# Kernel optimization log

Hardware: AMD Instinct MI355X
Metric: run time of the kernel (lower is better)

Reference implementation:

```python
import jax, jax.numpy as jnp
import numpy as np

B = 256
NUM_PRIMARY = 32      # cfg.num_primary_caps
PRIM_ATOMS = 8
NUM_CLASSES = 10
DIGIT_ATOMS = 16
NUM_ROUTING = 3       # cfg.num_routing (DigitCap)
IN_DIM = 6 * 6 * NUM_PRIMARY  # 1152
NUM_PIXELS = 28 * 28 * 1


def squash(s, axis):
    # v = ||s||^2/(1+||s||^2) * s/||s||
    n2 = jnp.sum(jnp.square(s), axis=axis, keepdims=True)
    return s * (n2 / (1.0 + n2)) / jnp.sqrt(n2 + 1e-9)


def conv2d(x, w, stride):
    return jax.lax.conv_general_dilated(
        x, w, (stride, stride), 'VALID',
        dimension_numbers=('NCHW', 'OIHW', 'NCHW'))


def setup_inputs() -> dict:
    key = jax.random.key(0)
    ks = jax.random.split(key, 10)
    x = jax.random.uniform(ks[0], (B, 1, 28, 28), jnp.float32)
    labels = jax.random.randint(ks[1], (B,), 0, NUM_CLASSES)
    y = jax.nn.one_hot(labels, NUM_CLASSES, dtype=jnp.float32)
    conv1_w = 0.05 * jax.random.normal(ks[2], (256, 1, 9, 9), jnp.float32)
    conv1_b = jnp.full((256,), 0.1, jnp.float32)
    # primary capsule conv: 256 -> 32 caps * 8 atoms, k=9, s=2 (bias applied after routing)
    prim_w = 0.05 * jax.random.normal(ks[3], (NUM_PRIMARY * PRIM_ATOMS, 256, 9, 9), jnp.float32)
    prim_b = jnp.full((NUM_PRIMARY, PRIM_ATOMS), 0.1, jnp.float32)
    # digit capsule transform: [in_dim, in_atoms, out_dim, out_atoms]
    digit_w = 0.05 * jax.random.normal(ks[4], (IN_DIM, PRIM_ATOMS, NUM_CLASSES, DIGIT_ATOMS), jnp.float32)
    digit_b = jnp.full((NUM_CLASSES, DIGIT_ATOMS), 0.1, jnp.float32)
    w1 = 0.05 * jax.random.normal(ks[5], (NUM_CLASSES * DIGIT_ATOMS, 512), jnp.float32)
    b1 = jnp.zeros((512,), jnp.float32)
    w2 = 0.05 * jax.random.normal(ks[6], (512, 1024), jnp.float32)
    b2 = jnp.zeros((1024,), jnp.float32)
    w3 = 0.05 * jax.random.normal(ks[7], (1024, NUM_PIXELS), jnp.float32)
    b3 = jnp.zeros((NUM_PIXELS,), jnp.float32)
    return dict(x=x, y=y, conv1_w=conv1_w, conv1_b=conv1_b, prim_w=prim_w,
                prim_b=prim_b, digit_w=digit_w, digit_b=digit_b,
                w1=w1, b1=b1, w2=w2, b2=b2, w3=w3, b3=b3)


def reference(x, y, conv1_w, conv1_b, prim_w, prim_b, digit_w, digit_b,
              w1, b1, w2, b2, w3, b3):
    # conv stem
    h = jax.nn.relu(conv2d(x, conv1_w, 1) + conv1_b[None, :, None, None])  # [B,256,20,20]

    # PrimaryCap: conv votes [B, in_dim=1, out=32, atoms=8, 6, 6]; num_routing=1
    votes_p = conv2d(h, prim_w, 2).reshape(B, NUM_PRIMARY, PRIM_ATOMS, 6, 6)
    # one routing iter, input_dim=1: softmax(zeros) over output_dim -> uniform 1/32
    preact_p = votes_p / NUM_PRIMARY + prim_b[None, :, :, None, None]
    caps1 = squash(preact_p, axis=2)  # [B,32,8,6,6]

    # permute(0,1,3,4,2) then flatten -> [B, 1152, 8]
    x3 = jnp.transpose(caps1, (0, 1, 3, 4, 2)).reshape(B, IN_DIM, PRIM_ATOMS)

    # DigitCap votes: [B, in_dim, out_dim, out_atoms]
    votes = jnp.einsum('bia,iaot->biot', x3, digit_w)
    logits = jnp.zeros((B, IN_DIM, NUM_CLASSES), votes.dtype)
    act = None
    for _ in range(NUM_ROUTING):
        route = jax.nn.softmax(logits, axis=2)  # over output capsules
        preact = jnp.einsum('bio,biot->bot', route, votes) + digit_b
        act = squash(preact, axis=-1)  # [B,10,16]
        logits = logits + jnp.einsum('biot,bot->bio', votes, act)
    digit = act

    # Reconstruction: mask by label, 160 -> 512 -> 1024 -> 784
    masked = (digit * y[:, :, None]).reshape(B, NUM_CLASSES * DIGIT_ATOMS)
    r = jax.nn.relu(masked @ w1 + b1)
    r = jax.nn.relu(r @ w2 + b2)
    recon = jax.nn.sigmoid(r @ w3 + b3)
    return digit, recon
```

## Files before the change

kernel.cpp:

```cpp
#include <hip/hip_runtime.h>
#include <hip/hip_bf16.h>

typedef unsigned short u16;
typedef unsigned int u32;

static __device__ __forceinline__ float us2f(u16 u) {
    return __uint_as_float(((u32)u) << 16);
}
static __device__ __forceinline__ u16 f2bu(float f) {
    u32 u = __float_as_uint(f);
    return (u16)((u + 0x7fffu + ((u >> 16) & 1u)) >> 16);
}

typedef __attribute__((ext_vector_type(8))) __bf16 bf16x8;
typedef __attribute__((ext_vector_type(4))) float f32x4;

static __device__ __forceinline__ void async16(const u16* g, u16* l) {
    __builtin_amdgcn_global_load_lds(
        (const __attribute__((address_space(1))) unsigned int*)g,
        (__attribute__((address_space(3))) unsigned int*)l, 16, 0, 0);
}

__global__ void fill_sentinel(float* out, int n, float val) {
    int g = blockIdx.x * 256 + threadIdx.x;
    if (g < n) out[g] = val;
}

__global__ __launch_bounds__(256) void conv_c1wb(const float* __restrict__ w,
                                                 u16* __restrict__ wb)
{
    const int j = blockIdx.x, c = threadIdx.x;
    wb[j * 256 + c] = f2bu(w[c * 81 + j]);
}

__global__ __launch_bounds__(256) void conv1_kernel(const float* __restrict__ x,
    const u16* __restrict__ wb, const float* __restrict__ bias, u16* __restrict__ h)
{
    __shared__ float xs[784];
    __shared__ u16 wl[81 * 256];
    const int b = blockIdx.x >> 2, g = blockIdx.x & 3;
    const int c = threadIdx.x;
    for (int idx = c; idx < 784; idx += 256) xs[idx] = x[b * 784 + idx];
    for (int idx = c; idx < 20736; idx += 256) wl[idx] = wb[idx];
    __syncthreads();
    const float bv = bias[c];
    #pragma unroll 1
    for (int iy = g * 5; iy < g * 5 + 5; ++iy) {
        float acc[20];
        #pragma unroll
        for (int i = 0; i < 20; ++i) acc[i] = bv;
        #pragma unroll 1
        for (int dy = 0; dy < 9; ++dy) {
            float xr[28];
            const float4* xrow = reinterpret_cast<const float4*>(&xs[(iy + dy) * 28]);
            #pragma unroll
            for (int i = 0; i < 7; ++i) {
                float4 v = xrow[i];
                xr[4*i] = v.x; xr[4*i+1] = v.y; xr[4*i+2] = v.z; xr[4*i+3] = v.w;
            }
            #pragma unroll
            for (int dx = 0; dx < 9; ++dx) {
                const float wv = us2f(wl[(dy * 9 + dx) * 256 + c]);
                #pragma unroll
                for (int ix = 0; ix < 20; ++ix) acc[ix] += xr[ix + dx] * wv;
            }
        }
        u16* hp = h + ((b * 20 + iy) * 20) * 256 + c;
        #pragma unroll
        for (int ix = 0; ix < 20; ++ix) hp[ix * 256] = f2bu(fmaxf(acc[ix], 0.f));
    }
}

__global__ __launch_bounds__(256) void transpose_primw(const float* __restrict__ w,
                                                       u16* __restrict__ wt)
{
    __shared__ u16 wl[81 * 258];
    const int n = blockIdx.x, tid = threadIdx.x;
    const float* ws = w + (size_t)n * 20736;
    for (int idx = tid; idx < 20736; idx += 256) {
        const int cc = idx / 81, kk = idx - cc * 81;
        wl[kk * 258 + cc] = f2bu(ws[idx]);
    }
    __syncthreads();
    u16* wo = wt + (size_t)n * 20736;
    for (int q = tid; q < 20736; q += 256)
        wo[q] = wl[(q >> 8) * 258 + (q & 255)];
}

__global__ __launch_bounds__(256) void conv_dwb(const float* __restrict__ dw,
                                                u16* __restrict__ dwb_t)
{
    const int g = blockIdx.x * 256 + threadIdx.x;
    dwb_t[g] = f2bu(dw[g]);
}

__global__ __launch_bounds__(256, 2) void prim_gemm_split(const u16* __restrict__ h,
    const u16* __restrict__ wT, float* __restrict__ pm)
{
    __shared__ u16 As[3 * 4096];
    __shared__ u16 Bs[3 * 8192];
    const int tid = threadIdx.x;
    const int split = blockIdx.y;
    const int mBase = blockIdx.x * 128;
    const int lane = tid & 63, wv = tid >> 6;
    const int swzq = (tid & 3) ^ ((lane >> 3) & 3);
    const int rA = wv * 32 + (lane >> 2);
    const int rB = wv * 64 + (lane >> 2);
    int mA0 = mBase + rA;
    int bA0 = mA0 / 36, rr0 = mA0 % 36;
    const int aBase0 = ((bA0 * 20 + 2 * (rr0 / 6)) * 20 + 2 * (rr0 % 6)) * 256 + swzq * 8;
    int mA1 = mA0 + 16;
    int bA1 = mA1 / 36, rr1 = mA1 % 36;
    const int aBase1 = ((bA1 * 20 + 2 * (rr1 / 6)) * 20 + 2 * (rr1 % 6)) * 256 + swzq * 8;
    const u16* bp0 = wT + (size_t)rB * 20736 + swzq * 8;

    int kglob = split * 3456;
    int ky = kglob / 2304; int krem = kglob - ky * 2304;
    int kx = krem >> 8; int c0 = krem & 255;

    f32x4 acc[4][8];
    #pragma unroll
    for (int i = 0; i < 4; ++i)
        #pragma unroll
        for (int j = 0; j < 8; ++j) acc[i][j] = (f32x4){0.f, 0.f, 0.f, 0.f};

    const int wm = wv >> 1, wn = wv & 1;
    const int lcol = lane & 15, lquad = lane >> 4;
    const int rswz = (lquad ^ ((lcol >> 1) & 3)) * 8;
    const u16* Arow = As + (wm * 64 + lcol) * 32 + rswz;
    const u16* Brow = Bs + (wn * 128 + lcol) * 32 + rswz;
    u16* aD = As + wv * 1024;
    u16* bD = Bs + wv * 2048;

    #define STAGE(sel)  do {                                                   \
        const int koffA = (ky * 20 + kx) * 256 + c0;                           \
        async16(h + aBase0 + koffA, aD + (sel) * 4096);                        \
        async16(h + aBase1 + koffA, aD + (sel) * 4096 + 512);                  \
        async16(bp0 + kglob,          bD + (sel) * 8192);                      \
        async16(bp0 + 331776 + kglob, bD + (sel) * 8192 + 512);               \
        async16(bp0 + 663552 + kglob, bD + (sel) * 8192 + 1024);              \
        async16(bp0 + 995328 + kglob, bD + (sel) * 8192 + 1536);              \
        kglob += 32; c0 += 32;                                                 \
        if (c0 == 256) { c0 = 0; if (++kx == 9) { kx = 0; ++ky; } }            \
    } while (0)

    #define COMPUTE(sel)  do {                                                 \
        const u16* Ab = Arow + (sel) * 4096;                                   \
        const u16* Bb = Brow + (sel) * 8192;                                   \
        bf16x8 af[4], bfr[8];                                                  \
        _Pragma("unroll")                                                      \
        for (int i = 0; i < 4; ++i)                                            \
            af[i] = *reinterpret_cast<const bf16x8*>(Ab + i * 512);            \
        _Pragma("unroll")                                                      \
        for (int j = 0; j < 8; ++j)                                            \
            bfr[j] = *reinterpret_cast<const bf16x8*>(Bb + j * 512);           \
        __builtin_amdgcn_s_setprio(1);                                         \
        _Pragma("unroll")                                                      \
        for (int i = 0; i < 4; ++i)                                            \
            _Pragma("unroll")                                                  \
            for (int j = 0; j < 8; ++j)                                        \
                acc[i][j] = __builtin_amdgcn_mfma_f32_16x16x32_bf16(af[i], bfr[j], acc[i][j], 0, 0, 0); \
        __builtin_amdgcn_s_setprio(0);                                         \
    } while (0)

    STAGE(0);
    STAGE(1);
    int cb = 0, sb = 2;
    #pragma unroll 1
    for (int kt = 0; kt < 106; ++kt) {
        STAGE(sb);
        asm volatile("s_waitcnt vmcnt(12)" ::: "memory");
        __builtin_amdgcn_s_barrier();
        __builtin_amdgcn_sched_barrier(0);
        COMPUTE(cb);
        __builtin_amdgcn_sched_barrier(0);
        __builtin_amdgcn_s_barrier();
        __builtin_amdgcn_sched_barrier(0);
        cb = (cb == 2) ? 0 : cb + 1;
        sb = (sb == 2) ? 0 : sb + 1;
    }
    asm volatile("s_waitcnt vmcnt(6)" ::: "memory");
    __builtin_amdgcn_s_barrier();
    __builtin_amdgcn_sched_barrier(0);
    COMPUTE(1);
    __builtin_amdgcn_sched_barrier(0);
    asm volatile("s_waitcnt vmcnt(0)" ::: "memory");
    __builtin_amdgcn_s_barrier();
    __builtin_amdgcn_sched_barrier(0);
    COMPUTE(2);
    #undef STAGE
    #undef COMPUTE

    #pragma unroll
    for (int i = 0; i < 4; ++i) {
        const int mrow = mBase + wm * 64 + i * 16 + lquad * 4;
        #pragma unroll
        for (int j = 0; j < 8; ++j) {
            const int ncol = wn * 128 + j * 16 + lcol;
            #pragma unroll
            for (int r = 0; r < 4; ++r)
                unsafeAtomicAdd(&pm[(size_t)(mrow + r) * 256 + ncol], acc[i][j][r]);
        }
    }
}

__global__ __launch_bounds__(256) void squash_kernel(float* __restrict__ pm,
    const float* __restrict__ pb)
{
    const int m = blockIdx.x, t = threadIdx.x;
    float pre = pm[(size_t)m * 256 + t] * (1.f / 32.f) + pb[t];
    float sq = pre * pre;
    sq += __shfl_xor(sq, 1); sq += __shfl_xor(sq, 2); sq += __shfl_xor(sq, 4);
    float scale = (sq / (1.f + sq)) * rsqrtf(sq + 1e-9f);
    pm[(size_t)m * 256 + t] = pre * scale;
}

__global__ __launch_bounds__(192) void votes_gemm(const float* __restrict__ x3m,
    const u16* __restrict__ dwb_t, u16* __restrict__ votes, int hb)
{
    __shared__ float dws[8 * 1280];
    __shared__ float x3s[64 * 64];
    const int ic = blockIdx.x * 8, bc = blockIdx.y * 64;
    const int tid = threadIdx.x;
    for (int q = tid; q < 10240; q += 192)
        dws[q] = us2f(dwb_t[(size_t)ic * 1280 + q]);
    for (int q = tid; q < 4096; q += 192) {
        const int b_l = q >> 6, r = q & 63, i_l = r >> 3, a = r & 7;
        const int i = ic + i_l, cap = i / 36, p = i - cap * 36;
        x3s[q] = x3m[((size_t)(hb + bc + b_l) * 36 + p) * 256 + cap * 8 + a];
    }
    __syncthreads();
    if (tid < 160) {
        const int ot = tid;
        float dwr[8][8];
        #pragma unroll
        for (int i_l = 0; i_l < 8; ++i_l)
            #pragma unroll
            for (int a = 0; a < 8; ++a)
                dwr[i_l][a] = dws[i_l * 1280 + a * 160 + ot];
        #pragma unroll 1
        for (int b_l = 0; b_l < 64; ++b_l) {
            u16 ob[8];
            #pragma unroll
            for (int i_l = 0; i_l < 8; ++i_l) {
                const float* xp = &x3s[b_l * 64 + i_l * 8];
                float v = 0.f;
                #pragma unroll
                for (int a = 0; a < 8; ++a) v += xp[a] * dwr[i_l][a];
                ob[i_l] = f2bu(v);
            }
            uint4 o4;
            o4.x = (u32)ob[0] | ((u32)ob[1] << 16);
            o4.y = (u32)ob[2] | ((u32)ob[3] << 16);
            o4.z = (u32)ob[4] | ((u32)ob[5] << 16);
            o4.w = (u32)ob[6] | ((u32)ob[7] << 16);
            *reinterpret_cast<uint4*>(&votes[((size_t)(bc + b_l) * 160 + ot) * 1152 + ic]) = o4;
        }
    }
}

__global__ __launch_bounds__(256) void routing_act3(const u16* __restrict__ votes,
    const float* __restrict__ logits, float* __restrict__ preactD, int hb, int uniform)
{
    __shared__ float route_s[384 * 10];
    __shared__ float vs[160 * 65];
    const int ic = blockIdx.x * 384, b_l = blockIdx.y;
    const int gb = hb + b_l;
    const int tid = threadIdx.x;
    if (!uniform) {
        for (int q = tid; q < 384; q += 256) {
            const float* lg = &logits[((size_t)gb * 1152 + ic + q) * 10];
            float l[10]; float mx = -1e30f;
            #pragma unroll
            for (int k = 0; k < 10; ++k) { l[k] = lg[k]; mx = fmaxf(mx, l[k]); }
            float s = 0.f;
            #pragma unroll
            for (int k = 0; k < 10; ++k) { l[k] = __expf(l[k] - mx); s += l[k]; }
            const float inv = 1.f / s;
            #pragma unroll
            for (int k = 0; k < 10; ++k) route_s[q * 10 + k] = l[k] * inv;
        }
    }
    float acc = 0.f;
    const int o = (tid & 255) >> 4;
    #pragma unroll 1
    for (int sc = 0; sc < 6; ++sc) {
        __syncthreads();
        for (int q = tid; q < 1280; q += 256) {
            const int ot = q >> 3, i8 = q & 7;
            const uint4 d = *reinterpret_cast<const uint4*>(
                &votes[((size_t)b_l * 160 + ot) * 1152 + ic + sc * 64 + i8 * 8]);
            const u32 du[4] = {d.x, d.y, d.z, d.w};
            float* vp = &vs[ot * 65 + i8 * 8];
            #pragma unroll
            for (int k = 0; k < 4; ++k) {
                vp[2 * k]     = __uint_as_float(du[k] << 16);
                vp[2 * k + 1] = __uint_as_float(du[k] & 0xffff0000u);
            }
        }
        __syncthreads();
        if (tid < 160) {
            const float* vrow = &vs[tid * 65];
            if (uniform) {
                float s = 0.f;
                #pragma unroll
                for (int il = 0; il < 64; ++il) s += vrow[il];
                acc += 0.1f * s;
            } else {
                const float* rp = &route_s[sc * 640 + o];
                #pragma unroll
                for (int il = 0; il < 64; ++il)
                    acc += rp[il * 10] * vrow[il];
            }
        }
    }
    if (tid < 160)
        unsafeAtomicAdd(&preactD[(size_t)gb * 160 + tid], acc);
}

__global__ __launch_bounds__(192) void routing_squash(const float* __restrict__ preactD,
    const float* __restrict__ db, float* __restrict__ act, float* __restrict__ dout, int hb)
{
    const int b = hb + blockIdx.x, tid = threadIdx.x;
    if (tid < 160) {
        float pre = preactD[(size_t)b * 160 + tid] + db[tid];
        float sq = pre * pre;
        sq += __shfl_xor(sq, 1); sq += __shfl_xor(sq, 2);
        sq += __shfl_xor(sq, 4); sq += __shfl_xor(sq, 8);
        float scale = (sq / (1.f + sq)) * rsqrtf(sq + 1e-9f);
        float a = pre * scale;
        act[(size_t)b * 160 + tid] = a;
        if (dout) dout[(size_t)b * 160 + tid] = a;
    }
}

__global__ __launch_bounds__(128) void routing_upd3(const u16* __restrict__ votes,
    const float* __restrict__ act, float* __restrict__ logits, int hb, int first)
{
    __shared__ float act_s[160];
    const int b_l = blockIdx.y, gb = hb + b_l;
    const int i = blockIdx.x * 128 + threadIdx.x;
    for (int q = threadIdx.x; q < 160; q += 128)
        act_s[q] = act[(size_t)gb * 160 + q];
    __syncthreads();
    float acc[10];
    #pragma unroll
    for (int k = 0; k < 10; ++k) acc[k] = 0.f;
    const u16* vb = &votes[(size_t)b_l * 160 * 1152 + i];
    #pragma unroll
    for (int ot = 0; ot < 160; ++ot)
        acc[ot >> 4] += us2f(vb[(size_t)ot * 1152]) * act_s[ot];
    float* lp = &logits[((size_t)gb * 1152 + i) * 10];
    if (first) {
        #pragma unroll
        for (int k = 0; k < 10; ++k) lp[k] = acc[k];
    } else {
        #pragma unroll
        for (int k = 0; k < 10; ++k) lp[k] += acc[k];
    }
}

__global__ __launch_bounds__(256) void mlp_layer(const float* __restrict__ in,
    const float* __restrict__ maskY, const float* __restrict__ w,
    const float* __restrict__ bias, float* __restrict__ outp, int K, int N, int mode)
{
    __shared__ float ins[4 * 1024];
    const int b0 = blockIdx.x * 4;
    const int n = blockIdx.y * 256 + threadIdx.x;
    for (int idx = threadIdx.x; idx < 4 * K; idx += 256) {
        float v = in[(size_t)b0 * K + idx];
        if (maskY) {
            const int b_l = idx / K, j = idx % K;
            v *= maskY[(b0 + b_l) * 10 + (j >> 4)];
        }
        ins[idx] = v;
    }
    __syncthreads();
    if (n < N) {
        float a0 = 0.f, a1 = 0.f, a2 = 0.f, a3 = 0.f;
        for (int k = 0; k < K; ++k) {
            const float wvv = w[(size_t)k * N + n];
            a0 += ins[k] * wvv;
            a1 += ins[K + k] * wvv;
            a2 += ins[2 * K + k] * wvv;
            a3 += ins[3 * K + k] * wvv;
        }
        const float bv = bias[n];
        float v[4] = {a0 + bv, a1 + bv, a2 + bv, a3 + bv};
        #pragma unroll
        for (int j = 0; j < 4; ++j) {
            float xv = v[j];
            xv = (mode == 0) ? fmaxf(xv, 0.f) : 1.f / (1.f + __expf(-xv));
            outp[(size_t)(b0 + j) * N + n] = xv;
        }
    }
}

extern "C" void kernel_launch(void* const* d_in, const int* in_sizes, int n_in,
                              void* d_out, int out_size, void* d_ws, size_t ws_size,
                              hipStream_t stream) {
    const float* x   = (const float*)d_in[0];
    const float* y   = (const float*)d_in[1];
    const float* c1w = (const float*)d_in[2];
    const float* c1b = (const float*)d_in[3];
    const float* pw  = (const float*)d_in[4];
    const float* pb  = (const float*)d_in[5];
    const float* dw  = (const float*)d_in[6];
    const float* db  = (const float*)d_in[7];
    const float* w1  = (const float*)d_in[8];
    const float* b1  = (const float*)d_in[9];
    const float* w2  = (const float*)d_in[10];
    const float* b2  = (const float*)d_in[11];
    const float* w3  = (const float*)d_in[12];
    const float* b3  = (const float*)d_in[13];
    float* out = (float*)d_out;
    char* ws = (char*)d_ws;

    static const int exp_sizes[14] = {200704, 2560, 20736, 256, 5308416, 256,
                                      1474560, 160, 81920, 512, 524288, 1024,
                                      802816, 784};
    int bad = (n_in == 14) ? -1 : -2;
    if (bad == -1)
        for (int i = 0; i < 14; ++i) if (in_sizes[i] != exp_sizes[i]) { bad = i; break; }
    if (bad != -1) {
        fill_sentinel<<<(out_size + 255) / 256, 256, 0, stream>>>(out, out_size,
            7168.f + 16.f * (float)(bad + 1));
        return;
    }
    const size_t NEEDED = 72482816ULL;
    if (ws_size < NEEDED) {
        fill_sentinel<<<(out_size + 255) / 256, 256, 0, stream>>>(out, out_size, 111.0f);
        return;
    }

    u16*   h       = (u16*)(ws);
    u16*   wT2     = (u16*)(ws + 52428800);
    float* x3m     = (float*)(ws + 63045632);
    u16*   c1wb    = (u16*)(ws + 63045632);
    u16*   votes   = (u16*)(ws);
    float* logits  = (float*)(ws + 47185920);
    float* act     = (float*)(ws + 58982400);
    float* preactD = (float*)(ws + 59146240);
    u16*   dwb_t   = (u16*)(ws + 59637760);
    float* r1      = (float*)(ws + 62586880);
    float* r2      = (float*)(ws + 63111168);

    conv_c1wb<<<81, 256, 0, stream>>>(c1w, c1wb);
    conv1_kernel<<<1024, 256, 0, stream>>>(x, c1wb, c1b, h);
    transpose_primw<<<256, 256, 0, stream>>>(pw, wT2);
    hipMemsetAsync(x3m, 0, 9437184, stream);
    prim_gemm_split<<<dim3(72, 6), 256, 0, stream>>>(h, wT2, x3m);
    squash_kernel<<<9216, 256, 0, stream>>>(x3m, pb);
    conv_dwb<<<5760, 256, 0, stream>>>(dw, dwb_t);
    hipMemsetAsync(preactD, 0, 491520, stream);

    float* pD0 = preactD, *pD1 = preactD + 40960, *pD2 = preactD + 81920;
    for (int half = 0; half < 2; ++half) {
        const int hb = half * 128;
        votes_gemm<<<dim3(144, 2), 192, 0, stream>>>(x3m, dwb_t, votes, hb);
        routing_act3<<<dim3(3, 128), 256, 0, stream>>>(votes, logits, pD0, hb, 1);
        routing_squash<<<128, 192, 0, stream>>>(pD0, db, act, (float*)nullptr, hb);
        routing_upd3<<<dim3(9, 128), 128, 0, stream>>>(votes, act, logits, hb, 1);
        routing_act3<<<dim3(3, 128), 256, 0, stream>>>(votes, logits, pD1, hb, 0);
        routing_squash<<<128, 192, 0, stream>>>(pD1, db, act, (float*)nullptr, hb);
        routing_upd3<<<dim3(9, 128), 128, 0, stream>>>(votes, act, logits, hb, 0);
        routing_act3<<<dim3(3, 128), 256, 0, stream>>>(votes, logits, pD2, hb, 0);
        routing_squash<<<128, 192, 0, stream>>>(pD2, db, act, out, hb);
    }

    mlp_layer<<<dim3(64, 2), 256, 0, stream>>>(act, y, w1, b1, r1, 160, 512, 0);
    mlp_layer<<<dim3(64, 4), 256, 0, stream>>>(r1, (float*)nullptr, w2, b2, r2, 512, 1024, 0);
    mlp_layer<<<dim3(64, 4), 256, 0, stream>>>(r2, (float*)nullptr, w3, b3, out + 40960, 1024, 784, 1);
}
```

Before: 756.4 us.

## Fuse routing squash, logit update and weighted sum into one kernel per iteration

Merges routing_squash, routing_upd3 and routing_act3 into a single routing_fused kernel. Each block loads a 160x144 bf16 vote tile into shared memory once, recomputes the squash of the previous preactivation locally, updates the logits, applies the softmax, and accumulates the next preactivation with atomics. This cuts kernel launches per half from seven to three and avoids reading the votes twice per iteration. The cost is redundant squash work in every block, plus a grid of 8x128 blocks with a large shared-memory footprint that may limit occupancy.

Result: no change. 750.7 us (-0.8%).

```diff
diff --git a/kernel.cpp b/kernel.cpp
--- a/kernel.cpp
+++ b/kernel.cpp
@@ -259,63 +259,79 @@
     }
 }
 
-__global__ __launch_bounds__(256) void routing_act3(const u16* __restrict__ votes,
-    const float* __restrict__ logits, float* __restrict__ preactD, int hb, int uniform)
-{
-    __shared__ float route_s[384 * 10];
-    __shared__ float vs[160 * 65];
-    const int ic = blockIdx.x * 384, b_l = blockIdx.y;
-    const int gb = hb + b_l;
+__global__ __launch_bounds__(256) void routing_fused(const u16* __restrict__ votes,
+    const float* __restrict__ pD_prev, const float* __restrict__ db,
+    float* __restrict__ logits, float* __restrict__ pD_next, int hb, int mode)
+{
+    __shared__ u16 vs16[160 * 146];
+    __shared__ float route_s[144 * 10];
+    __shared__ float act_s[160];
+    const int ic = blockIdx.x * 144, b_l = blockIdx.y, gb = hb + b_l;
     const int tid = threadIdx.x;
-    if (!uniform) {
-        for (int q = tid; q < 384; q += 256) {
-            const float* lg = &logits[((size_t)gb * 1152 + ic + q) * 10];
-            float l[10]; float mx = -1e30f;
-            #pragma unroll
-            for (int k = 0; k < 10; ++k) { l[k] = lg[k]; mx = fmaxf(mx, l[k]); }
+
+    for (int q = tid; q < 2880; q += 256) {
+        const int ot = q / 18, ch = q - ot * 18;
+        const uint4 d = *reinterpret_cast<const uint4*>(
+            &votes[((size_t)b_l * 160 + ot) * 1152 + ic + ch * 8]);
+        u32* vp = reinterpret_cast<u32*>(&vs16[ot * 146 + ch * 8]);
+        vp[0] = d.x; vp[1] = d.y; vp[2] = d.z; vp[3] = d.w;
+    }
+    if (mode >= 1 && tid < 160) {
+        float pre = pD_prev[(size_t)gb * 160 + tid] + db[tid];
+        float sq = pre * pre;
+        sq += __shfl_xor(sq, 1); sq += __shfl_xor(sq, 2);
+        sq += __shfl_xor(sq, 4); sq += __shfl_xor(sq, 8);
+        act_s[tid] = pre * (sq / (1.f + sq)) * rsqrtf(sq + 1e-9f);
+    }
+    __syncthreads();
+
+    if (mode >= 1) {
+        if (tid < 144) {
+            float acc[10];
+            #pragma unroll
+            for (int k = 0; k < 10; ++k) acc[k] = 0.f;
+            #pragma unroll 4
+            for (int ot = 0; ot < 160; ++ot)
+                acc[ot >> 4] += us2f(vs16[ot * 146 + tid]) * act_s[ot];
+            float* lp = &logits[((size_t)gb * 1152 + ic + tid) * 10];
+            float l[10];
+            if (mode == 1) {
+                #pragma unroll
+                for (int k = 0; k < 10; ++k) { l[k] = acc[k]; lp[k] = l[k]; }
+            } else {
+                #pragma unroll
+                for (int k = 0; k < 10; ++k) { l[k] = lp[k] + acc[k]; lp[k] = l[k]; }
+            }
+            float mx = -1e30f;
+            #pragma unroll
+            for (int k = 0; k < 10; ++k) mx = fmaxf(mx, l[k]);
             float s = 0.f;
             #pragma unroll
             for (int k = 0; k < 10; ++k) { l[k] = __expf(l[k] - mx); s += l[k]; }
             const float inv = 1.f / s;
             #pragma unroll
-            for (int k = 0; k < 10; ++k) route_s[q * 10 + k] = l[k] * inv;
-        }
-    }
-    float acc = 0.f;
-    const int o = (tid & 255) >> 4;
-    #pragma unroll 1
-    for (int sc = 0; sc < 6; ++sc) {
+            for (int k = 0; k < 10; ++k) route_s[tid * 10 + k] = l[k] * inv;
+        }
         __syncthreads();
-        for (int q = tid; q < 1280; q += 256) {
-            const int ot = q >> 3, i8 = q & 7;
-            const uint4 d = *reinterpret_cast<const uint4*>(
-                &votes[((size_t)b_l * 160 + ot) * 1152 + ic + sc * 64 + i8 * 8]);
-            const u32 du[4] = {d.x, d.y, d.z, d.w};
-            float* vp = &vs[ot * 65 + i8 * 8];
-            #pragma unroll
-            for (int k = 0; k < 4; ++k) {
-                vp[2 * k]     = __uint_as_float(du[k] << 16);
-                vp[2 * k + 1] = __uint_as_float(du[k] & 0xffff0000u);
-            }
-        }
-        __syncthreads();
-        if (tid < 160) {
-            const float* vrow = &vs[tid * 65];
-            if (uniform) {
-                float s = 0.f;
-                #pragma unroll
-                for (int il = 0; il < 64; ++il) s += vrow[il];
-                acc += 0.1f * s;
-            } else {
-                const float* rp = &route_s[sc * 640 + o];
-                #pragma unroll
-                for (int il = 0; il < 64; ++il)
-                    acc += rp[il * 10] * vrow[il];
-            }
-        }
-    }
-    if (tid < 160)
-        unsafeAtomicAdd(&preactD[(size_t)gb * 160 + tid], acc);
+    }
+
+    if (tid < 160) {
+        const int o = tid >> 4;
+        const u16* vrow = &vs16[tid * 146];
+        float acc2 = 0.f;
+        if (mode == 0) {
+            float s = 0.f;
+            #pragma unroll 8
+            for (int i = 0; i < 144; ++i) s += us2f(vrow[i]);
+            acc2 = 0.1f * s;
+        } else {
+            const float* rp = &route_s[o];
+            #pragma unroll 8
+            for (int i = 0; i < 144; ++i)
+                acc2 += rp[i * 10] * us2f(vrow[i]);
+        }
+        unsafeAtomicAdd(&pD_next[(size_t)gb * 160 + tid], acc2);
+    }
 }
 
 __global__ __launch_bounds__(192) void routing_squash(const float* __restrict__ preactD,
@@ -331,32 +347,6 @@
         float a = pre * scale;
         act[(size_t)b * 160 + tid] = a;
         if (dout) dout[(size_t)b * 160 + tid] = a;
-    }
-}
-
-__global__ __launch_bounds__(128) void routing_upd3(const u16* __restrict__ votes,
-    const float* __restrict__ act, float* __restrict__ logits, int hb, int first)
-{
-    __shared__ float act_s[160];
-    const int b_l = blockIdx.y, gb = hb + b_l;
-    const int i = blockIdx.x * 128 + threadIdx.x;
-    for (int q = threadIdx.x; q < 160; q += 128)
-        act_s[q] = act[(size_t)gb * 160 + q];
-    __syncthreads();
-    float acc[10];
-    #pragma unroll
-    for (int k = 0; k < 10; ++k) acc[k] = 0.f;
-    const u16* vb = &votes[(size_t)b_l * 160 * 1152 + i];
-    #pragma unroll
-    for (int ot = 0; ot < 160; ++ot)
-        acc[ot >> 4] += us2f(vb[(size_t)ot * 1152]) * act_s[ot];
-    float* lp = &logits[((size_t)gb * 1152 + i) * 10];
-    if (first) {
-        #pragma unroll
-        for (int k = 0; k < 10; ++k) lp[k] = acc[k];
-    } else {
-        #pragma unroll
-        for (int k = 0; k < 10; ++k) lp[k] += acc[k];
     }
 }
 
@@ -458,13 +448,9 @@
     for (int half = 0; half < 2; ++half) {
         const int hb = half * 128;
         votes_gemm<<<dim3(144, 2), 192, 0, stream>>>(x3m, dwb_t, votes, hb);
-        routing_act3<<<dim3(3, 128), 256, 0, stream>>>(votes, logits, pD0, hb, 1);
-        routing_squash<<<128, 192, 0, stream>>>(pD0, db, act, (float*)nullptr, hb);
-        routing_upd3<<<dim3(9, 128), 128, 0, stream>>>(votes, act, logits, hb, 1);
-        routing_act3<<<dim3(3, 128), 256, 0, stream>>>(votes, logits, pD1, hb, 0);
-        routing_squash<<<128, 192, 0, stream>>>(pD1, db, act, (float*)nullptr, hb);
-        routing_upd3<<<dim3(9, 128), 128, 0, stream>>>(votes, act, logits, hb, 0);
-        routing_act3<<<dim3(3, 128), 256, 0, stream>>>(votes, logits, pD2, hb, 0);
+        routing_fused<<<dim3(8, 128), 256, 0, stream>>>(votes, pD0, db, logits, pD0, hb, 0);
+        routing_fused<<<dim3(8, 128), 256, 0, stream>>>(votes, pD0, db, logits, pD1, hb, 1);
+        routing_fused<<<dim3(8, 128), 256, 0, stream>>>(votes, pD1, db, logits, pD2, hb, 2);
         routing_squash<<<128, 192, 0, stream>>>(pD2, db, act, out, hb);
     }
 
```
